# Optimization experiments

Measured on AMD Instinct MI355X. Metric: run time of the kernel, lower is better.

## Reference

```python
import jax, jax.numpy as jnp
import numpy as np

B, S, H, D = 4, 1024, 16, 128
E = H * D  # 2048
TOTAL = B * S
NUM_SLOTS = 2 * TOTAL


def setup_inputs() -> dict:
    key = jax.random.key(0)
    k1, k2, k3, k4, k5 = jax.random.split(key, 5)
    return {
        "hidden_states": jax.random.normal(k1, (TOTAL, E), dtype=jnp.float32) * 0.02,
        "c_attn_w": jax.random.normal(k2, (E, 3 * E), dtype=jnp.float32) * 0.02,
        "c_attn_b": jax.random.normal(k3, (3 * E,), dtype=jnp.float32) * 0.02,
        "c_proj_w": jax.random.normal(k4, (E, E), dtype=jnp.float32) * 0.02,
        "c_proj_b": jax.random.normal(k5, (E,), dtype=jnp.float32) * 0.02,
        "key_cache": jnp.zeros((NUM_SLOTS, H, D), dtype=jnp.float32),
        "value_cache": jnp.zeros((NUM_SLOTS, H, D), dtype=jnp.float32),
        "slots": jnp.arange(TOTAL, dtype=jnp.int32),
        "seq_len": S,
    }


def reference(hidden_states, c_attn_w, c_attn_b, c_proj_w, c_proj_b,
              key_cache, value_cache, slots, seq_len):
    total, embed = hidden_states.shape
    n_heads, head_dim = key_cache.shape[1], key_cache.shape[2]
    b = total // seq_len

    # fused QKV projection (fan_in_fan_out: y = x @ W + b)
    qkv = hidden_states @ c_attn_w + c_attn_b            # [total, 3E]
    qkv = qkv.reshape(total, 3, n_heads, head_dim)
    q, k, v = qkv[:, 0], qkv[:, 1], qkv[:, 2]

    # paged_attention.reshape_and_cache: scatter new k/v into the paged cache
    key_cache = key_cache.at[slots].set(k)
    value_cache = value_cache.at[slots].set(v)
    # prefill attention reads current tokens' k/v (gathered back from cache)
    k = key_cache[slots]
    v = value_cache[slots]

    # varlen causal flash attention over b equal-length sequences
    qb = q.reshape(b, seq_len, n_heads, head_dim)
    kb = k.reshape(b, seq_len, n_heads, head_dim)
    vb = v.reshape(b, seq_len, n_heads, head_dim)
    scale = jnp.asarray(head_dim, qb.dtype) ** -0.5       # softmax_scale
    scores = jnp.einsum("bqhd,bkhd->bhqk", qb, kb) * scale
    causal = jnp.tril(jnp.ones((seq_len, seq_len), dtype=bool))
    scores = jnp.where(causal, scores, jnp.finfo(scores.dtype).min)
    attn = jax.nn.softmax(scores, axis=-1)
    ctx = jnp.einsum("bhqk,bkhd->bqhd", attn, vb)
    ctx = ctx.reshape(total, embed)

    # output projection (fan_in_fan_out row-parallel linear)
    out = ctx @ c_proj_w + c_proj_b
    return out
```

## Files before the change

kernel.cpp:

```cpp
#include <hip/hip_runtime.h>
#include <stdint.h>

typedef __bf16 bf16x8 __attribute__((ext_vector_type(8)));
typedef float  f32x4  __attribute__((ext_vector_type(4)));

#define DEV static __device__ __forceinline__

DEV unsigned short f2bf(float x) {
    union { float f; unsigned int u; } v; v.f = x;
    unsigned int r = v.u + 0x7FFFu + ((v.u >> 16) & 1u);
    return (unsigned short)(r >> 16);
}

DEV void gl_lds16(const void* g, void* l) {
    __builtin_amdgcn_global_load_lds(
        (__attribute__((address_space(1))) void*)(g),
        (__attribute__((address_space(3))) void*)(l), 16, 0, 0);
}

DEV f32x4 zero4() { f32x4 z; z[0]=0.f; z[1]=0.f; z[2]=0.f; z[3]=0.f; return z; }

__global__ void k_cvt_bf16(const float* __restrict__ in, unsigned short* __restrict__ out, int n) {
    int i = (blockIdx.x * blockDim.x + threadIdx.x) * 4;
    int stride = gridDim.x * blockDim.x * 4;
    for (; i < n; i += stride) {
        float4 f = *(const float4*)(in + i);
        ushort4 o;
        o.x = f2bf(f.x); o.y = f2bf(f.y); o.z = f2bf(f.z); o.w = f2bf(f.w);
        *(ushort4*)(out + i) = o;
    }
}

__global__ void k_transpose_bf16(const float* __restrict__ in, unsigned short* __restrict__ out,
                                 int K, int N) {
    __shared__ float tile[32][33];
    int n0 = blockIdx.x * 32, k0 = blockIdx.y * 32;
    int tx = threadIdx.x, ty = threadIdx.y;
    #pragma unroll
    for (int i = 0; i < 4; i++)
        tile[ty + i*8][tx] = in[(size_t)(k0 + ty + i*8) * N + n0 + tx];
    __syncthreads();
    #pragma unroll
    for (int i = 0; i < 4; i++)
        out[(size_t)(n0 + ty + i*8) * K + k0 + tx] = f2bf(tile[tx][ty + i*8]);
}

template<int MODE>
__launch_bounds__(256, 2)
__global__ void k_gemm(const unsigned short* __restrict__ A,
                       const unsigned short* __restrict__ BT,
                       const float* __restrict__ bias,
                       float* __restrict__ outp,
                       unsigned short* __restrict__ q_buf,
                       unsigned short* __restrict__ k_buf,
                       unsigned short* __restrict__ vt_buf,
                       int M, int N, int K) {
    __shared__ __align__(16) uint4 As[128*8];
    __shared__ __align__(16) uint4 Bs[128*8];

    const int t = threadIdx.x;
    const int wave = t >> 6, lane = t & 63, quad = lane >> 4, l15 = lane & 15;
    const int wm = wave & 1, wn = wave >> 1;
    const int bm = blockIdx.x, bn = blockIdx.y;

    f32x4 acc[4][4];
    #pragma unroll
    for (int i = 0; i < 4; i++)
        #pragma unroll
        for (int j = 0; j < 4; j++) acc[i][j] = zero4();

    int rS[4], gS[4];
    #pragma unroll
    for (int p = 0; p < 4; p++) {
        int c = p*4 + wave;
        int s = c*64 + lane;
        int r = s >> 3;
        rS[p] = r; gS[p] = (lane & 7) ^ (r & 7);
    }
    const unsigned short* Abase = A  + (size_t)(bm*128) * K;
    const unsigned short* Bbase = BT + (size_t)(bn*128) * K;

    const int kiters = K >> 6;
    for (int kk = 0; kk < kiters; kk++) {
        const int k0 = kk * 64;
        __syncthreads();
        #pragma unroll
        for (int p = 0; p < 4; p++) {
            int c = p*4 + wave;
            gl_lds16(Abase + (size_t)rS[p]*K + k0 + gS[p]*8, &As[c*64]);
            gl_lds16(Bbase + (size_t)rS[p]*K + k0 + gS[p]*8, &Bs[c*64]);
        }
        __syncthreads();
        #pragma unroll
        for (int ks = 0; ks < 2; ks++) {
            bf16x8 af[4], bfr[4];
            #pragma unroll
            for (int mt = 0; mt < 4; mt++) {
                int row = wm*64 + mt*16 + l15;
                int g = (ks*4 + quad) ^ (row & 7);
                af[mt] = __builtin_bit_cast(bf16x8, As[row*8 + g]);
            }
            #pragma unroll
            for (int nt = 0; nt < 4; nt++) {
                int row = wn*64 + nt*16 + l15;
                int g = (ks*4 + quad) ^ (row & 7);
                bfr[nt] = __builtin_bit_cast(bf16x8, Bs[row*8 + g]);
            }
            #pragma unroll
            for (int mt = 0; mt < 4; mt++)
                #pragma unroll
                for (int nt = 0; nt < 4; nt++)
                    acc[mt][nt] = __builtin_amdgcn_mfma_f32_16x16x32_bf16(
                        af[mt], bfr[nt], acc[mt][nt], 0, 0, 0);
        }
    }

    if (MODE == 1) {
        #pragma unroll
        for (int nt = 0; nt < 4; nt++) {
            int n = bn*128 + wn*64 + nt*16 + l15;
            float bv = bias[n];
            #pragma unroll
            for (int mt = 0; mt < 4; mt++) {
                int m = bm*128 + wm*64 + mt*16 + quad*4;
                #pragma unroll
                for (int r = 0; r < 4; r++)
                    outp[(size_t)(m + r) * N + n] = acc[mt][nt][r] + bv;
            }
        }
    } else {
        const int nglob = bn * 128;
        const int seg = nglob >> 11;
        const int cn_base = (nglob & 2047) + wn*64;
        if (seg < 2) {
            unsigned short* dst = (seg == 0) ? q_buf : k_buf;
            const float scl = (seg == 0) ? 0.08838834764831845f : 1.0f;
            #pragma unroll
            for (int nt = 0; nt < 4; nt++) {
                int cn = cn_base + nt*16 + l15;
                float bv = bias[nglob + wn*64 + nt*16 + l15];
                #pragma unroll
                for (int mt = 0; mt < 4; mt++) {
                    int tt = bm*128 + wm*64 + mt*16 + quad*4;
                    #pragma unroll
                    for (int r = 0; r < 4; r++)
                        dst[(size_t)(tt + r) * 2048 + cn] = f2bf((acc[mt][nt][r] + bv) * scl);
                }
            }
        } else {
            #pragma unroll
            for (int nt = 0; nt < 4; nt++) {
                int cn = cn_base + nt*16 + l15;
                int h = cn >> 7, d = cn & 127;
                float bv = bias[nglob + wn*64 + nt*16 + l15];
                #pragma unroll
                for (int mt = 0; mt < 4; mt++) {
                    int tt = bm*128 + wm*64 + mt*16 + quad*4;
                    int b = tt >> 10, s = tt & 1023;
                    ushort4 pk;
                    pk.x = f2bf(acc[mt][nt][0] + bv);
                    pk.y = f2bf(acc[mt][nt][1] + bv);
                    pk.z = f2bf(acc[mt][nt][2] + bv);
                    pk.w = f2bf(acc[mt][nt][3] + bv);
                    *(ushort4*)(vt_buf + ((size_t)((b*16 + h)*128 + d) * 1024 + s)) = pk;
                }
            }
        }
    }
}

__launch_bounds__(256, 2)
__global__ void k_attn(const unsigned short* __restrict__ q_buf,
                       const unsigned short* __restrict__ k_buf,
                       const unsigned short* __restrict__ vt_buf,
                       unsigned short* __restrict__ ctx_buf) {
    __shared__ __align__(16) uint4 Ks[64*16];
    __shared__ __align__(16) uint4 Vs[128*8];
    __shared__ __align__(16) unsigned short Pl[4][16*64];

    const int t = threadIdx.x;
    const int wave = t >> 6, lane = t & 63, quad = lane >> 4, l15 = lane & 15;
    const int qt = (int)gridDim.x - 1 - (int)blockIdx.x;
    const int bh = blockIdx.y;
    const int b = bh >> 4, h = bh & 15;

    const size_t qoff = (size_t)(b*1024 + qt*64 + wave*16 + l15) * 2048 + h*128;
    bf16x8 qf[4];
    #pragma unroll
    for (int ks = 0; ks < 4; ks++)
        qf[ks] = __builtin_bit_cast(bf16x8, *(const uint4*)(q_buf + qoff + ks*32 + quad*8));

    f32x4 ctx[8];
    #pragma unroll
    for (int i = 0; i < 8; i++) ctx[i] = zero4();
    float m_run[4], l_run[4];
    #pragma unroll
    for (int r = 0; r < 4; r++) { m_run[r] = -__builtin_inff(); l_run[r] = 0.f; }

    const size_t kbase = (size_t)b * 1024 * 2048 + h*128;
    const size_t vbase = (size_t)(b*16 + h) * 131072;

    for (int kt = 0; kt <= qt; kt++) {
        __syncthreads();
        #pragma unroll
        for (int p = 0; p < 4; p++) {
            int c = p*4 + wave;
            {
                int s = c*64 + lane;
                int r = s >> 4;
                int g = (s & 15) ^ (r & 15);
                gl_lds16(k_buf + kbase + (size_t)(kt*64 + r) * 2048 + g*8, &Ks[c*64]);
            }
            {
                int s = c*64 + lane;
                int r = s >> 3;
                int g = (lane & 7) ^ (r & 7);
                gl_lds16(vt_buf + vbase + (size_t)r * 1024 + kt*64 + g*8, &Vs[c*64]);
            }
        }
        __syncthreads();

        f32x4 sacc[4];
        #pragma unroll
        for (int nt = 0; nt < 4; nt++) sacc[nt] = zero4();
        #pragma unroll
        for (int ks = 0; ks < 4; ks++)
            #pragma unroll
            for (int nt = 0; nt < 4; nt++) {
                int key = nt*16 + l15;
                int g = (ks*4 + quad) ^ (key & 15);
                bf16x8 kf = __builtin_bit_cast(bf16x8, Ks[key*16 + g]);
                sacc[nt] = __builtin_amdgcn_mfma_f32_16x16x32_bf16(qf[ks], kf, sacc[nt], 0, 0, 0);
            }

        float sv[4][4];
        #pragma unroll
        for (int nt = 0; nt < 4; nt++)
            #pragma unroll
            for (int r = 0; r < 4; r++) sv[nt][r] = sacc[nt][r];
        if (kt == qt) {
            #pragma unroll
            for (int nt = 0; nt < 4; nt++)
                #pragma unroll
                for (int r = 0; r < 4; r++)
                    if (nt*16 + l15 > wave*16 + quad*4 + r) sv[nt][r] = -__builtin_inff();
        }

        float alpha[4], pv[4][4];
        #pragma unroll
        for (int r = 0; r < 4; r++) {
            float mr = fmaxf(fmaxf(sv[0][r], sv[1][r]), fmaxf(sv[2][r], sv[3][r]));
            mr = fmaxf(mr, __shfl_xor(mr, 1));
            mr = fmaxf(mr, __shfl_xor(mr, 2));
            mr = fmaxf(mr, __shfl_xor(mr, 4));
            mr = fmaxf(mr, __shfl_xor(mr, 8));
            float mn = fmaxf(m_run[r], mr);
            alpha[r] = __expf(m_run[r] - mn);
            m_run[r] = mn;
            float s0 = __expf(sv[0][r] - mn), s1 = __expf(sv[1][r] - mn);
            float s2 = __expf(sv[2][r] - mn), s3 = __expf(sv[3][r] - mn);
            pv[0][r] = s0; pv[1][r] = s1; pv[2][r] = s2; pv[3][r] = s3;
            float rs = (s0 + s1) + (s2 + s3);
            rs += __shfl_xor(rs, 1);
            rs += __shfl_xor(rs, 2);
            rs += __shfl_xor(rs, 4);
            rs += __shfl_xor(rs, 8);
            l_run[r] = l_run[r] * alpha[r] + rs;
        }
        #pragma unroll
        for (int dt = 0; dt < 8; dt++)
            #pragma unroll
            for (int r = 0; r < 4; r++) ctx[dt][r] *= alpha[r];

        #pragma unroll
        for (int nt = 0; nt < 4; nt++)
            #pragma unroll
            for (int r = 0; r < 4; r++) {
                int row = quad*4 + r;
                int col = nt*16 + l15;
                int gc = (col >> 3) ^ (row & 7);
                Pl[wave][row*64 + gc*8 + (col & 7)] = f2bf(pv[nt][r]);
            }
        __asm__ volatile("s_waitcnt lgkmcnt(0)" ::: "memory");

        #pragma unroll
        for (int ks = 0; ks < 2; ks++) {
            int gp = (ks*4 + quad) ^ (l15 & 7);
            bf16x8 pa = __builtin_bit_cast(bf16x8, *(const uint4*)&Pl[wave][l15*64 + gp*8]);
            #pragma unroll
            for (int dt = 0; dt < 8; dt++) {
                int drow = dt*16 + l15;
                int gv = (ks*4 + quad) ^ (drow & 7);
                bf16x8 vf = __builtin_bit_cast(bf16x8, Vs[drow*8 + gv]);
                ctx[dt] = __builtin_amdgcn_mfma_f32_16x16x32_bf16(pa, vf, ctx[dt], 0, 0, 0);
            }
        }
    }

    float inv[4];
    #pragma unroll
    for (int r = 0; r < 4; r++) inv[r] = 1.0f / l_run[r];
    const int tt0 = b*1024 + qt*64 + wave*16 + quad*4;
    #pragma unroll
    for (int dt = 0; dt < 8; dt++)
        #pragma unroll
        for (int r = 0; r < 4; r++)
            ctx_buf[(size_t)(tt0 + r) * 2048 + h*128 + dt*16 + l15] = f2bf(ctx[dt][r] * inv[r]);
}

extern "C" void kernel_launch(void* const* d_in, const int* in_sizes, int n_in,
                              void* d_out, int out_size, void* d_ws, size_t ws_size,
                              hipStream_t stream) {
    const float* hs    = (const float*)d_in[0];
    const float* wqkv  = (const float*)d_in[1];
    const float* bqkv  = (const float*)d_in[2];
    const float* wproj = (const float*)d_in[3];
    const float* bproj = (const float*)d_in[4];

    char* ws = (char*)d_ws;
    unsigned short* hs_bf   = (unsigned short*)(ws);
    unsigned short* wqkvT   = (unsigned short*)(ws + 16777216ull);
    unsigned short* wprojT  = (unsigned short*)(ws + 41943040ull);
    unsigned short* q_buf   = (unsigned short*)(ws + 50331648ull);
    unsigned short* k_buf   = (unsigned short*)(ws + 67108864ull);
    unsigned short* vt_buf  = (unsigned short*)(ws + 83886080ull);
    unsigned short* ctx_buf = (unsigned short*)(ws + 100663296ull);

    k_cvt_bf16<<<2048, 256, 0, stream>>>(hs, hs_bf, 4096 * 2048);
    k_transpose_bf16<<<dim3(6144/32, 2048/32), dim3(32, 8), 0, stream>>>(wqkv, wqkvT, 2048, 6144);
    k_transpose_bf16<<<dim3(2048/32, 2048/32), dim3(32, 8), 0, stream>>>(wproj, wprojT, 2048, 2048);

    k_gemm<0><<<dim3(32, 48), 256, 0, stream>>>(hs_bf, wqkvT, bqkv, nullptr,
                                                q_buf, k_buf, vt_buf, 4096, 6144, 2048);
    k_attn<<<dim3(16, 64), 256, 0, stream>>>(q_buf, k_buf, vt_buf, ctx_buf);
    k_gemm<1><<<dim3(32, 16), 256, 0, stream>>>(ctx_buf, wprojT, bproj, (float*)d_out,
                                                nullptr, nullptr, nullptr, 4096, 2048, 2048);
}
```

Before: 432.1 us.

## Double attention query tile per block to 128 rows and reorder grid

Each attention block now handles 128 query rows, with each wave owning two 16-row subtiles, so every K/V tile loaded into LDS is reused across twice as many queries. This halves the number of blocks and cuts redundant K/V loads. Waves whose rows sit entirely above a key tile skip its compute, though they still take part in the shared loads and barriers. The grid is reordered so heads run along x and query tiles along y, and the GEMM launch bound is raised to 4 blocks per CU, which may cost registers or cause spills.

```diff
diff --git a/kernel.cpp b/kernel.cpp
--- a/kernel.cpp
+++ b/kernel.cpp
@@ -46,7 +46,7 @@
 }
 
 template<int MODE>
-__launch_bounds__(256, 2)
+__launch_bounds__(256, 4)
 __global__ void k_gemm(const unsigned short* __restrict__ A,
                        const unsigned short* __restrict__ BT,
                        const float* __restrict__ bias,
@@ -176,31 +176,40 @@
                        unsigned short* __restrict__ ctx_buf) {
     __shared__ __align__(16) uint4 Ks[64*16];
     __shared__ __align__(16) uint4 Vs[128*8];
-    __shared__ __align__(16) unsigned short Pl[4][16*64];
+    __shared__ __align__(16) unsigned short Pl[4][32*64];
 
     const int t = threadIdx.x;
     const int wave = t >> 6, lane = t & 63, quad = lane >> 4, l15 = lane & 15;
-    const int qt = (int)gridDim.x - 1 - (int)blockIdx.x;
-    const int bh = blockIdx.y;
+    const int qt = 7 - (int)blockIdx.y;
+    const int bh = blockIdx.x;
     const int b = bh >> 4, h = bh & 15;
 
-    const size_t qoff = (size_t)(b*1024 + qt*64 + wave*16 + l15) * 2048 + h*128;
-    bf16x8 qf[4];
-    #pragma unroll
-    for (int ks = 0; ks < 4; ks++)
-        qf[ks] = __builtin_bit_cast(bf16x8, *(const uint4*)(q_buf + qoff + ks*32 + quad*8));
-
-    f32x4 ctx[8];
-    #pragma unroll
-    for (int i = 0; i < 8; i++) ctx[i] = zero4();
-    float m_run[4], l_run[4];
-    #pragma unroll
-    for (int r = 0; r < 4; r++) { m_run[r] = -__builtin_inff(); l_run[r] = 0.f; }
+    bf16x8 qf[2][4];
+    #pragma unroll
+    for (int rt = 0; rt < 2; rt++) {
+        const size_t qoff = (size_t)(b*1024 + qt*128 + wave*32 + rt*16 + l15) * 2048 + h*128;
+        #pragma unroll
+        for (int ks = 0; ks < 4; ks++)
+            qf[rt][ks] = __builtin_bit_cast(bf16x8, *(const uint4*)(q_buf + qoff + ks*32 + quad*8));
+    }
+
+    f32x4 ctx[2][8];
+    #pragma unroll
+    for (int rt = 0; rt < 2; rt++)
+        #pragma unroll
+        for (int i = 0; i < 8; i++) ctx[rt][i] = zero4();
+    float m_run[2][4], l_run[2][4];
+    #pragma unroll
+    for (int rt = 0; rt < 2; rt++)
+        #pragma unroll
+        for (int r = 0; r < 4; r++) { m_run[rt][r] = -__builtin_inff(); l_run[rt][r] = 0.f; }
 
     const size_t kbase = (size_t)b * 1024 * 2048 + h*128;
     const size_t vbase = (size_t)(b*16 + h) * 131072;
-
-    for (int kt = 0; kt <= qt; kt++) {
+    const int row0 = qt*128 + wave*32;
+
+    const int kiters = 2*qt + 2;
+    for (int kt = 0; kt < kiters; kt++) {
         __syncthreads();
         #pragma unroll
         for (int p = 0; p < 4; p++) {
@@ -220,92 +229,105 @@
         }
         __syncthreads();
 
-        f32x4 sacc[4];
-        #pragma unroll
-        for (int nt = 0; nt < 4; nt++) sacc[nt] = zero4();
-        #pragma unroll
-        for (int ks = 0; ks < 4; ks++)
-            #pragma unroll
-            for (int nt = 0; nt < 4; nt++) {
-                int key = nt*16 + l15;
-                int g = (ks*4 + quad) ^ (key & 15);
-                bf16x8 kf = __builtin_bit_cast(bf16x8, Ks[key*16 + g]);
-                sacc[nt] = __builtin_amdgcn_mfma_f32_16x16x32_bf16(qf[ks], kf, sacc[nt], 0, 0, 0);
-            }
-
-        float sv[4][4];
-        #pragma unroll
-        for (int nt = 0; nt < 4; nt++)
-            #pragma unroll
-            for (int r = 0; r < 4; r++) sv[nt][r] = sacc[nt][r];
-        if (kt == qt) {
+        if (kt*64 > row0 + 31) continue;
+        const bool needmask = (kt*64 + 63 > row0);
+
+        #pragma unroll
+        for (int rt = 0; rt < 2; rt++) {
+            f32x4 sacc[4];
+            #pragma unroll
+            for (int nt = 0; nt < 4; nt++) sacc[nt] = zero4();
+            #pragma unroll
+            for (int ks = 0; ks < 4; ks++)
+                #pragma unroll
+                for (int nt = 0; nt < 4; nt++) {
+                    int key = nt*16 + l15;
+                    int g = (ks*4 + quad) ^ (key & 15);
+                    bf16x8 kf = __builtin_bit_cast(bf16x8, Ks[key*16 + g]);
+                    sacc[nt] = __builtin_amdgcn_mfma_f32_16x16x32_bf16(qf[rt][ks], kf, sacc[nt], 0, 0, 0);
+                }
+
+            float sv[4][4];
             #pragma unroll
             for (int nt = 0; nt < 4; nt++)
                 #pragma unroll
-                for (int r = 0; r < 4; r++)
-                    if (nt*16 + l15 > wave*16 + quad*4 + r) sv[nt][r] = -__builtin_inff();
-        }
-
-        float alpha[4], pv[4][4];
-        #pragma unroll
-        for (int r = 0; r < 4; r++) {
-            float mr = fmaxf(fmaxf(sv[0][r], sv[1][r]), fmaxf(sv[2][r], sv[3][r]));
-            mr = fmaxf(mr, __shfl_xor(mr, 1));
-            mr = fmaxf(mr, __shfl_xor(mr, 2));
-            mr = fmaxf(mr, __shfl_xor(mr, 4));
-            mr = fmaxf(mr, __shfl_xor(mr, 8));
-            float mn = fmaxf(m_run[r], mr);
-            alpha[r] = __expf(m_run[r] - mn);
-            m_run[r] = mn;
-            float s0 = __expf(sv[0][r] - mn), s1 = __expf(sv[1][r] - mn);
-            float s2 = __expf(sv[2][r] - mn), s3 = __expf(sv[3][r] - mn);
-            pv[0][r] = s0; pv[1][r] = s1; pv[2][r] = s2; pv[3][r] = s3;
-            float rs = (s0 + s1) + (s2 + s3);
-            rs += __shfl_xor(rs, 1);
-            rs += __shfl_xor(rs, 2);
-            rs += __shfl_xor(rs, 4);
-            rs += __shfl_xor(rs, 8);
-            l_run[r] = l_run[r] * alpha[r] + rs;
-        }
+                for (int r = 0; r < 4; r++) sv[nt][r] = sacc[nt][r];
+            if (needmask) {
+                #pragma unroll
+                for (int nt = 0; nt < 4; nt++)
+                    #pragma unroll
+                    for (int r = 0; r < 4; r++)
+                        if (kt*64 + nt*16 + l15 > row0 + rt*16 + quad*4 + r)
+                            sv[nt][r] = -__builtin_inff();
+            }
+
+            float alpha[4], pv[4][4];
+            #pragma unroll
+            for (int r = 0; r < 4; r++) {
+                float mr = fmaxf(fmaxf(sv[0][r], sv[1][r]), fmaxf(sv[2][r], sv[3][r]));
+                mr = fmaxf(mr, __shfl_xor(mr, 1));
+                mr = fmaxf(mr, __shfl_xor(mr, 2));
+                mr = fmaxf(mr, __shfl_xor(mr, 4));
+                mr = fmaxf(mr, __shfl_xor(mr, 8));
+                float mn = fmaxf(m_run[rt][r], mr);
+                alpha[r] = __expf(m_run[rt][r] - mn);
+                m_run[rt][r] = mn;
+                float s0 = __expf(sv[0][r] - mn), s1 = __expf(sv[1][r] - mn);
+                float s2 = __expf(sv[2][r] - mn), s3 = __expf(sv[3][r] - mn);
+                pv[0][r] = s0; pv[1][r] = s1; pv[2][r] = s2; pv[3][r] = s3;
+                float rs = (s0 + s1) + (s2 + s3);
+                rs += __shfl_xor(rs, 1);
+                rs += __shfl_xor(rs, 2);
+                rs += __shfl_xor(rs, 4);
+                rs += __shfl_xor(rs, 8);
+                l_run[rt][r] = l_run[rt][r] * alpha[r] + rs;
+            }
+            #pragma unroll
+            for (int dt = 0; dt < 8; dt++)
+                #pragma unroll
+                for (int r = 0; r < 4; r++) ctx[rt][dt][r] *= alpha[r];
+
+            #pragma unroll
+            for (int nt = 0; nt < 4; nt++)
+                #pragma unroll
+                for (int r = 0; r < 4; r++) {
+                    int row = rt*16 + quad*4 + r;
+                    int col = nt*16 + l15;
+                    int gc = (col >> 3) ^ (row & 7);
+                    Pl[wave][row*64 + gc*8 + (col & 7)] = f2bf(pv[nt][r]);
+                }
+        }
+        __asm__ volatile("s_waitcnt lgkmcnt(0)" ::: "memory");
+
+        #pragma unroll
+        for (int rt = 0; rt < 2; rt++)
+            #pragma unroll
+            for (int ks = 0; ks < 2; ks++) {
+                int row = rt*16 + l15;
+                int gp = (ks*4 + quad) ^ (row & 7);
+                bf16x8 pa = __builtin_bit_cast(bf16x8, *(const uint4*)&Pl[wave][row*64 + gp*8]);
+                #pragma unroll
+                for (int dt = 0; dt < 8; dt++) {
+                    int drow = dt*16 + l15;
+                    int gv = (ks*4 + quad) ^ (drow & 7);
+                    bf16x8 vf = __builtin_bit_cast(bf16x8, Vs[drow*8 + gv]);
+                    ctx[rt][dt] = __builtin_amdgcn_mfma_f32_16x16x32_bf16(pa, vf, ctx[rt][dt], 0, 0, 0);
+                }
+            }
+    }
+
+    #pragma unroll
+    for (int rt = 0; rt < 2; rt++) {
+        float inv[4];
+        #pragma unroll
+        for (int r = 0; r < 4; r++) inv[r] = 1.0f / l_run[rt][r];
+        const int tt0 = b*1024 + qt*128 + wave*32 + rt*16 + quad*4;
         #pragma unroll
         for (int dt = 0; dt < 8; dt++)
             #pragma unroll
-            for (int r = 0; r < 4; r++) ctx[dt][r] *= alpha[r];
-
-        #pragma unroll
-        for (int nt = 0; nt < 4; nt++)
-            #pragma unroll
-            for (int r = 0; r < 4; r++) {
-                int row = quad*4 + r;
-                int col = nt*16 + l15;
-                int gc = (col >> 3) ^ (row & 7);
-                Pl[wave][row*64 + gc*8 + (col & 7)] = f2bf(pv[nt][r]);
-            }
-        __asm__ volatile("s_waitcnt lgkmcnt(0)" ::: "memory");
-
-        #pragma unroll
-        for (int ks = 0; ks < 2; ks++) {
-            int gp = (ks*4 + quad) ^ (l15 & 7);
-            bf16x8 pa = __builtin_bit_cast(bf16x8, *(const uint4*)&Pl[wave][l15*64 + gp*8]);
-            #pragma unroll
-            for (int dt = 0; dt < 8; dt++) {
-                int drow = dt*16 + l15;
-                int gv = (ks*4 + quad) ^ (drow & 7);
-                bf16x8 vf = __builtin_bit_cast(bf16x8, Vs[drow*8 + gv]);
-                ctx[dt] = __builtin_amdgcn_mfma_f32_16x16x32_bf16(pa, vf, ctx[dt], 0, 0, 0);
-            }
-        }
-    }
-
-    float inv[4];
-    #pragma unroll
-    for (int r = 0; r < 4; r++) inv[r] = 1.0f / l_run[r];
-    const int tt0 = b*1024 + qt*64 + wave*16 + quad*4;
-    #pragma unroll
-    for (int dt = 0; dt < 8; dt++)
-        #pragma unroll
-        for (int r = 0; r < 4; r++)
-            ctx_buf[(size_t)(tt0 + r) * 2048 + h*128 + dt*16 + l15] = f2bf(ctx[dt][r] * inv[r]);
+            for (int r = 0; r < 4; r++)
+                ctx_buf[(size_t)(tt0 + r) * 2048 + h*128 + dt*16 + l15] = f2bf(ctx[rt][dt][r] * inv[r]);
+    }
 }
 
 extern "C" void kernel_launch(void* const* d_in, const int* in_sizes, int n_in,
@@ -332,7 +354,7 @@
 
     k_gemm<0><<<dim3(32, 48), 256, 0, stream>>>(hs_bf, wqkvT, bqkv, nullptr,
                                                 q_buf, k_buf, vt_buf, 4096, 6144, 2048);
-    k_attn<<<dim3(16, 64), 256, 0, stream>>>(q_buf, k_buf, vt_buf, ctx_buf);
+    k_attn<<<dim3(64, 8), 256, 0, stream>>>(q_buf, k_buf, vt_buf, ctx_buf);
     k_gemm<1><<<dim3(32, 16), 256, 0, stream>>>(ctx_buf, wprojT, bproj, (float*)d_out,
                                                 nullptr, nullptr, nullptr, 4096, 2048, 2048);
 }
```

Result: no change. 427.2 us (-1.1%).
